# Performance work log

Measured on AMD Instinct MI355X. Metric: run time of the kernel, lower is better.

Reference implementation:

```python
import jax, jax.numpy as jnp
import numpy as np

# Config from Hyperparameters / __init__ args
B, S, D = 2, 2048, 512
H, KV, HD = 8, 4, 64          # num_heads, num_kv_heads, head_dim = D // H
ROPE_BASE = 10000.0
QK_GAIN_INIT = 1.5
EPS = 1e-6


def setup_inputs() -> dict:
    key = jax.random.key(0)
    k0, k1, k2, k3, k4 = jax.random.split(key, 5)
    std = 0.02
    return {
        "x": jax.random.normal(k0, (B, S, D), dtype=jnp.float32),
        "wq": jax.random.normal(k1, (H * HD, D), dtype=jnp.float32) * std,
        "wk": jax.random.normal(k2, (KV * HD, D), dtype=jnp.float32) * std,
        "wv": jax.random.normal(k3, (KV * HD, D), dtype=jnp.float32) * std,
        "wo": jax.random.normal(k4, (D, H * HD), dtype=jnp.float32) * std,
        "qk_gain": jnp.asarray(QK_GAIN_INIT, dtype=jnp.float32),
    }


def _rope_tables(seq_len, head_dim, base, dtype):
    inv_freq = 1.0 / (base ** (jnp.arange(0, head_dim, 2, dtype=jnp.float32) / head_dim))
    t = jnp.arange(seq_len, dtype=jnp.float32)
    freqs = t[:, None] * inv_freq[None, :]              # [S, HD/2]
    return jnp.cos(freqs).astype(dtype)[None, None], jnp.sin(freqs).astype(dtype)[None, None]


def _apply_rotary(x, cos, sin):
    # matches apply_rotary_emb: split halves, rotate
    half = x.shape[-1] // 2
    x1, x2 = x[..., :half], x[..., half:]
    return jnp.concatenate([x1 * cos + x2 * sin, x1 * (-sin) + x2 * cos], axis=-1)


def _rms_norm(u):
    return u * jax.lax.rsqrt(jnp.mean(u * u, axis=-1, keepdims=True) + EPS)


def reference(x, wq, wk, wv, wo, qk_gain):
    b, s, d = x.shape
    # fused-style QKV projections (CastedLinear, no bias)
    q = (x @ wq.T).reshape(b, s, H, HD).transpose(0, 2, 1, 3)    # [B,H,S,HD]
    k = (x @ wk.T).reshape(b, s, KV, HD).transpose(0, 2, 1, 3)   # [B,KV,S,HD]
    v = (x @ wv.T).reshape(b, s, KV, HD).transpose(0, 2, 1, 3)   # [B,KV,S,HD]

    cos, sin = _rope_tables(s, HD, ROPE_BASE, x.dtype)
    q = _apply_rotary(q, cos, sin)
    k = _apply_rotary(k, cos, sin)

    # QK RMS-norm with learnable gain (init 1.5) on q
    q = _rms_norm(q) * qk_gain
    k = _rms_norm(k)

    # GQA: expand KV heads to H query heads
    rep = H // KV
    k = jnp.repeat(k, rep, axis=1)   # [B,H,S,HD]
    v = jnp.repeat(v, rep, axis=1)

    scale = 1.0 / np.sqrt(HD)
    scores = jnp.einsum("bhqd,bhkd->bhqk", q, k) * scale         # [B,H,S,S]
    causal = jnp.tril(jnp.ones((s, s), dtype=bool))
    scores = jnp.where(causal, scores, jnp.finfo(scores.dtype).min)
    attn = jax.nn.softmax(scores, axis=-1)
    out = jnp.einsum("bhqk,bhkd->bhqd", attn, v)                 # [B,H,S,HD]
    out = out.transpose(0, 2, 1, 3).reshape(b, s, H * HD)
    return out @ wo.T
```

## Files before the change

### kernel.cpp

```cpp
#include <hip/hip_runtime.h>
#include <math.h>

#define B_ 2
#define S_ 2048
#define D_ 512
#define H_ 8
#define KV_ 4
#define HD_ 64

typedef __attribute__((ext_vector_type(8))) short bf16x8;
typedef __attribute__((ext_vector_type(4))) short bf16x4;
typedef __attribute__((ext_vector_type(4))) float f32x4;
typedef __attribute__((ext_vector_type(16))) float f32x16;
typedef __attribute__((ext_vector_type(4))) unsigned u32x4;

static __device__ __forceinline__ unsigned short f2bf(float f) {
    union { float f; unsigned u; } v; v.f = f;
    unsigned r = v.u + 0x7FFFu + ((v.u >> 16) & 1);
    return (unsigned short)(r >> 16);
}

__global__ __launch_bounds__(256) void convert_pack_kernel(
    const float* __restrict__ x, const float* __restrict__ wq, const float* __restrict__ wk,
    const float* __restrict__ wv, const float* __restrict__ wo,
    unsigned short* __restrict__ xb, unsigned short* __restrict__ wqkv_b,
    unsigned short* __restrict__ wo_b, float* __restrict__ cosT, float* __restrict__ sinT) {
    if (blockIdx.x >= 2816) {
        int idx = (blockIdx.x - 2816) * 256 + threadIdx.x;
        int s = idx >> 5;
        int i = idx & 31;
        float invf = 1.0f / powf(10000.0f, (float)(2 * i) / (float)HD_);
        double a = (double)((float)s * invf);
        cosT[idx] = (float)cos(a);
        sinT[idx] = (float)sin(a);
        return;
    }
    int i4 = blockIdx.x * blockDim.x + threadIdx.x;
    int e = i4 * 4;
    const float* src;
    unsigned short* dst;
    if (e < 2097152)      { src = x + e;               dst = xb + e; }
    else if (e < 2359296) { src = wq + (e - 2097152);  dst = wqkv_b + (e - 2097152); }
    else if (e < 2490368) { src = wk + (e - 2359296);  dst = wqkv_b + (e - 2097152); }
    else if (e < 2621440) { src = wv + (e - 2490368);  dst = wqkv_b + (e - 2097152); }
    else                  { src = wo + (e - 2621440);  dst = wo_b + (e - 2621440); }
    float4 v = *(const float4*)src;
    bf16x4 o;
    o[0] = (short)f2bf(v.x); o[1] = (short)f2bf(v.y);
    o[2] = (short)f2bf(v.z); o[3] = (short)f2bf(v.w);
    *(bf16x4*)dst = o;
}

template <int EPI, typename OutT>
static __device__ __forceinline__ void gemm_body(
    const unsigned short* __restrict__ A, const unsigned short* __restrict__ Bw,
    OutT* __restrict__ Y, int K, int ldy, int bn, int bm,
    unsigned short* As, unsigned short* Bs,
    const float* __restrict__ cosT, const float* __restrict__ sinT,
    const float* __restrict__ gainp) {
    const int t = threadIdx.x;
    const int w = t >> 6, l = t & 63;
    const int g = l >> 4, c = l & 15;
    const int wr = w >> 1, wc = w & 1;
    f32x4 acc[4][4] = {};
    const int lrow = l >> 2;
    const int lcol = (l & 3) * 8;
    for (int k0 = 0; k0 < K; k0 += 32) {
#pragma unroll
        for (int r = 0; r < 2; ++r) {
            int ci = w * 2 + r;
            const unsigned short* ga = A + (size_t)(bm + ci * 16 + lrow) * K + k0 + lcol;
            __builtin_amdgcn_global_load_lds(
                (const __attribute__((address_space(1))) void*)ga,
                (__attribute__((address_space(3))) void*)(As + ci * 512), 16, 0, 0);
            const unsigned short* gb = Bw + (size_t)(bn + ci * 16 + lrow) * K + k0 + lcol;
            __builtin_amdgcn_global_load_lds(
                (const __attribute__((address_space(1))) void*)gb,
                (__attribute__((address_space(3))) void*)(Bs + ci * 512), 16, 0, 0);
        }
        __syncthreads();
        bf16x8 av[4], bv[4];
#pragma unroll
        for (int i = 0; i < 4; ++i)
            av[i] = *(const bf16x8*)(As + (wr * 64 + i * 16 + c) * 32 + g * 8);
#pragma unroll
        for (int j = 0; j < 4; ++j)
            bv[j] = *(const bf16x8*)(Bs + (wc * 64 + j * 16 + c) * 32 + g * 8);
#pragma unroll
        for (int i = 0; i < 4; ++i)
#pragma unroll
            for (int j = 0; j < 4; ++j)
                acc[i][j] = __builtin_amdgcn_mfma_f32_16x16x32_bf16(av[i], bv[j], acc[i][j], 0, 0, 0);
        __syncthreads();
    }
    if constexpr (EPI == 2) {
        const float gv = *gainp;
        const float hscale = ((bn + wc * 64) < 512) ? gv : 1.0f;
#pragma unroll
        for (int i = 0; i < 4; ++i) {
#pragma unroll
            for (int r = 0; r < 4; ++r) {
                int row = bm + wr * 64 + i * 16 + g * 4 + r;
                int s = row & (S_ - 1);
                float c0 = cosT[s * 32 + c],      s0 = sinT[s * 32 + c];
                float c1 = cosT[s * 32 + c + 16], s1 = sinT[s * 32 + c + 16];
                float x1a = acc[i][0][r], x1b = acc[i][1][r];
                float x2a = acc[i][2][r], x2b = acc[i][3][r];
                float y1a = x1a * c0 + x2a * s0, y2a = x2a * c0 - x1a * s0;
                float y1b = x1b * c1 + x2b * s1, y2b = x2b * c1 - x1b * s1;
                float ss = y1a * y1a + y2a * y2a + y1b * y1b + y2b * y2b;
                ss += __shfl_xor(ss, 1, 64);
                ss += __shfl_xor(ss, 2, 64);
                ss += __shfl_xor(ss, 4, 64);
                ss += __shfl_xor(ss, 8, 64);
                float sc = rsqrtf(ss * (1.0f / 64.0f) + 1e-6f) * hscale;
                unsigned short* yr = (unsigned short*)Y + (size_t)row * ldy + bn + wc * 64 + c;
                yr[0]  = f2bf(y1a * sc);
                yr[16] = f2bf(y1b * sc);
                yr[32] = f2bf(y2a * sc);
                yr[48] = f2bf(y2b * sc);
            }
        }
    } else {
#pragma unroll
        for (int i = 0; i < 4; ++i)
#pragma unroll
            for (int j = 0; j < 4; ++j)
#pragma unroll
                for (int r = 0; r < 4; ++r) {
                    int row = bm + wr * 64 + i * 16 + g * 4 + r;
                    int col = bn + wc * 64 + j * 16 + c;
                    float v = acc[i][j][r];
                    if constexpr (EPI == 1)
                        Y[(size_t)row * ldy + col] = (OutT)f2bf(v);
                    else
                        Y[(size_t)row * ldy + col] = v;
                }
    }
}

__global__ __launch_bounds__(256) void gemm_proj_fused(
    const unsigned short* __restrict__ xb, const unsigned short* __restrict__ wqkv_b,
    unsigned short* __restrict__ qkv, unsigned short* __restrict__ vt,
    const float* __restrict__ cosT, const float* __restrict__ sinT,
    const float* __restrict__ gainp) {
    __shared__ unsigned short As[128 * 32];
    __shared__ unsigned short Bs[128 * 32];
    int bid = blockIdx.x;
    if (bid < 192) {
        int bx = bid % 6, by = bid / 6;
        gemm_body<2, unsigned short>(xb, wqkv_b, qkv, 512, 768, bx * 128, by * 128,
                                     As, Bs, cosT, sinT, gainp);
    } else {
        int b2 = bid - 192;
        int bx = b2 & 31, by = b2 >> 5;
        gemm_body<1, unsigned short>(wqkv_b + 768 * 512, xb, vt, 512, 4096, bx * 128, by * 128,
                                     As, Bs, nullptr, nullptr, nullptr);
    }
}

__global__ __launch_bounds__(256) void gemm_out(
    const unsigned short* __restrict__ A, const unsigned short* __restrict__ Bw,
    float* __restrict__ Y) {
    __shared__ unsigned short As[128 * 32];
    __shared__ unsigned short Bs[128 * 32];
    gemm_body<0, float>(A, Bw, Y, 512, 512, blockIdx.x % 4 * 128, blockIdx.x / 4 * 128,
                        As, Bs, nullptr, nullptr, nullptr);
}

#define SWZF(row) ((((row) + ((row) >> 3)) & 7) << 4)

__global__ __launch_bounds__(256, 3) void attn_mfma(const unsigned short* __restrict__ qkv,
                                                    const unsigned short* __restrict__ vt,
                                                    unsigned short* __restrict__ aout,
                                                    float* __restrict__ pO,
                                                    float* __restrict__ pL) {
    __shared__ alignas(128) char smem[32768];

    const int slot = blockIdx.x >> 4;
    const int bh = blockIdx.x & 15;
    int qt = 31, acc = 0;
    while (acc + (qt >> 3) + 1 <= slot) { acc += (qt >> 3) + 1; --qt; }
    const int part = slot - acc;
    const int np = (qt >> 3) + 1;
    const int kt0 = part * 8;
    const int kt1 = min(kt0 + 8, qt + 1);
    const int hh = bh & 7;
    const int b = bh >> 3;
    const int kvh = hh >> 1;

    const int t = threadIdx.x;
    const int w = t >> 6;
    const int l = t & 63;
    const int wq = w >> 1;
    const int wk = w & 1;
    const int hl = l >> 5;
    const int l31 = l & 31;

    const int row0 = t >> 3;
    const int row1 = (256 + t) >> 3;
    const int seg = l & 7;
    const int off0 = (seg * 16) ^ SWZF(row0);
    const int off1 = (seg * 16) ^ SWZF(row1);
    const int cb0 = w * 1024;
    const int cb1 = 4096 + w * 1024;

    bf16x8 qf[4];
    {
        const unsigned short* qrow =
            qkv + (size_t)(b * S_ + qt * 64 + wq * 32 + l31) * 768 + hh * 64 + hl * 8;
#pragma unroll
        for (int kd = 0; kd < 4; ++kd)
            qf[kd] = *(const bf16x8*)(qrow + kd * 16);
    }

    const char* kb = (const char*)qkv + ((size_t)(b * S_)) * 1536 + 1024 + kvh * 128;
    const char* vb = (const char*)vt + ((size_t)(kvh * 64)) * 8192 + (size_t)(b * S_) * 2;

#define STAGE(kt_, bufi_)                                                                        \
    do {                                                                                         \
        const char* ks_ = kb + (size_t)(kt_) * 64 * 1536;                                        \
        const char* vs_ = vb + (size_t)(kt_) * 128;                                              \
        char* kd_ = smem + (bufi_)*8192;                                                         \
        char* vd_ = smem + 16384 + (bufi_)*8192;                                                 \
        __builtin_amdgcn_global_load_lds(                                                        \
            (const __attribute__((address_space(1))) void*)(ks_ + (size_t)row0 * 1536 + off0),   \
            (__attribute__((address_space(3))) void*)(kd_ + cb0), 16, 0, 0);                     \
        __builtin_amdgcn_global_load_lds(                                                        \
            (const __attribute__((address_space(1))) void*)(ks_ + (size_t)row1 * 1536 + off1),   \
            (__attribute__((address_space(3))) void*)(kd_ + cb1), 16, 0, 0);                     \
        __builtin_amdgcn_global_load_lds(                                                        \
            (const __attribute__((address_space(1))) void*)(vs_ + (size_t)row0 * 8192 + off0),   \
            (__attribute__((address_space(3))) void*)(vd_ + cb0), 16, 0, 0);                     \
        __builtin_amdgcn_global_load_lds(                                                        \
            (const __attribute__((address_space(1))) void*)(vs_ + (size_t)row1 * 8192 + off1),   \
            (__attribute__((address_space(3))) void*)(vd_ + cb1), 16, 0, 0);                     \
    } while (0)

    STAGE(kt0, 0);
    __syncthreads();

    float l_part = 0.0f;
    f32x16 o_acc[2] = {};
    const float LS = 0.125f * 1.4426950408889634f;
    const float SH = 6.0f * 1.4426950408889634f;

    int buf = 0;
    for (int kt = kt0; kt < kt1; ++kt) {
        if (kt + 1 < kt1) STAGE(kt + 1, buf ^ 1);
        const char* KsB = smem + buf * 8192;
        const char* VtB = smem + 16384 + buf * 8192;
        const bool diag = (kt == qt);

        if (!(diag && wk > wq)) {
            f32x16 s_acc = {};
            {
                int arow = wk * 32 + l31;
                int af = SWZF(arow);
                __builtin_amdgcn_s_setprio(1);
#pragma unroll
                for (int kd = 0; kd < 4; ++kd) {
                    bf16x8 afr = *(const bf16x8*)(KsB + arow * 128 + ((kd * 32 + hl * 16) ^ af));
                    s_acc = __builtin_amdgcn_mfma_f32_32x32x16_bf16(afr, qf[kd], s_acc, 0, 0, 0);
                }
                __builtin_amdgcn_s_setprio(0);
            }
            bf16x8 vf[2][2];
#pragma unroll
            for (int nd = 0; nd < 2; ++nd) {
                int vr = nd * 32 + l31;
                int fv = SWZF(vr);
#pragma unroll
                for (int m = 0; m < 2; ++m)
                    vf[nd][m] = *(const bf16x8*)(VtB + vr * 128 + ((wk * 64 + m * 32 + hl * 16) ^ fv));
            }
            float p[16];
            if (diag && wk == wq) {
#pragma unroll
                for (int idx = 0; idx < 16; ++idx) {
                    int keyin = 4 * hl + 8 * (idx >> 2) + (idx & 3);
                    float e = exp2f(s_acc[idx] * LS - SH);
                    p[idx] = (keyin <= l31) ? e : 0.0f;
                }
            } else {
#pragma unroll
                for (int idx = 0; idx < 16; ++idx)
                    p[idx] = exp2f(s_acc[idx] * LS - SH);
            }
#pragma unroll
            for (int idx = 0; idx < 16; ++idx) l_part += p[idx];
            unsigned pw[8];
#pragma unroll
            for (int s = 0; s < 4; ++s)
#pragma unroll
                for (int j = 0; j < 2; ++j)
                    asm("v_cvt_pk_bf16_f32 %0, %1, %2"
                        : "=v"(pw[s * 2 + j])
                        : "v"(p[4 * s + 2 * j]), "v"(p[4 * s + 2 * j + 1]));
#pragma unroll
            for (int m = 0; m < 2; ++m) {
                asm volatile("v_permlane32_swap_b32 %0, %1" : "+v"(pw[4 * m + 0]), "+v"(pw[4 * m + 2]));
                asm volatile("v_permlane32_swap_b32 %0, %1" : "+v"(pw[4 * m + 1]), "+v"(pw[4 * m + 3]));
            }
            __builtin_amdgcn_s_setprio(1);
#pragma unroll
            for (int m = 0; m < 2; ++m) {
                u32x4 fu = {pw[4 * m + 0], pw[4 * m + 1], pw[4 * m + 2], pw[4 * m + 3]};
                bf16x8 pfr = *(bf16x8*)&fu;
#pragma unroll
                for (int nd = 0; nd < 2; ++nd)
                    o_acc[nd] = __builtin_amdgcn_mfma_f32_32x32x16_bf16(pfr, vf[nd][m], o_acc[nd], 0, 0, 0);
            }
            __builtin_amdgcn_s_setprio(0);
        }
        __syncthreads();
        buf ^= 1;
    }
#undef STAGE

    float* Os = (float*)smem;
    float* Ls = (float*)(smem + 16384);
    float lsum = l_part + __shfl_xor(l_part, 32, 64);
    if (hl == 0) Ls[wk * 64 + wq * 32 + l31] = lsum;
    if (wk == 0) {
#pragma unroll
        for (int nd = 0; nd < 2; ++nd)
#pragma unroll
            for (int reg = 0; reg < 16; ++reg) {
                int qrow = 4 * hl + 8 * (reg >> 2) + (reg & 3);
                Os[(wq * 32 + qrow) * 64 + nd * 32 + l31] = o_acc[nd][reg];
            }
    }
    __syncthreads();
    if (wk == 1) {
        if (np == 1) {
            unsigned short* ob = aout + ((size_t)(b * S_ + qt * 64 + wq * 32)) * 512 + hh * 64;
#pragma unroll
            for (int reg = 0; reg < 16; ++reg) {
                int qrow = 4 * hl + 8 * (reg >> 2) + (reg & 3);
                float ltot = Ls[wq * 32 + qrow] + Ls[64 + wq * 32 + qrow];
                float inv = __builtin_amdgcn_rcpf(ltot);
#pragma unroll
                for (int nd = 0; nd < 2; ++nd) {
                    float val = (o_acc[nd][reg] + Os[(wq * 32 + qrow) * 64 + nd * 32 + l31]) * inv;
                    ob[(size_t)qrow * 512 + nd * 32 + l31] = f2bf(val);
                }
            }
        } else {
            float* po = pO + (size_t)blockIdx.x * 4096;
            float* pl = pL + (size_t)blockIdx.x * 64;
#pragma unroll
            for (int reg = 0; reg < 16; ++reg) {
                int qrow = 4 * hl + 8 * (reg >> 2) + (reg & 3);
                float ltot = Ls[wq * 32 + qrow] + Ls[64 + wq * 32 + qrow];
                if (l31 == 0) pl[wq * 32 + qrow] = ltot;
#pragma unroll
                for (int nd = 0; nd < 2; ++nd)
                    po[(wq * 32 + qrow) * 64 + nd * 32 + l31] =
                        o_acc[nd][reg] + Os[(wq * 32 + qrow) * 64 + nd * 32 + l31];
            }
        }
    }
}

__global__ __launch_bounds__(256) void combine_kernel(const float* __restrict__ pO,
                                                      const float* __restrict__ pL,
                                                      unsigned short* __restrict__ aout) {
    const int cid = blockIdx.x;
    const int bh = cid & 15;
    const int qt = 31 - (cid >> 4);
    int qq = 31, acc = 0;
    while (qq > qt) { acc += (qq >> 3) + 1; --qq; }
    const int np = (qt >> 3) + 1;
    const int base = acc * 16 + bh;
    const int t = threadIdx.x;
    const int row = t >> 2;
    const int c0 = (t & 3) * 16;
    float l = 0.0f;
    float o[16] = {};
    for (int p = 0; p < np; ++p) {
        const int pid = base + p * 16;
        l += pL[(size_t)pid * 64 + row];
        const float* po = pO + (size_t)pid * 4096 + row * 64 + c0;
#pragma unroll
        for (int j4 = 0; j4 < 4; ++j4) {
            float4 v = *(const float4*)(po + j4 * 4);
            o[j4 * 4 + 0] += v.x; o[j4 * 4 + 1] += v.y;
            o[j4 * 4 + 2] += v.z; o[j4 * 4 + 3] += v.w;
        }
    }
    float inv = __builtin_amdgcn_rcpf(l);
    const int b = bh >> 3, hh = bh & 7;
    unsigned short* ob = aout + (size_t)(b * S_ + qt * 64 + row) * 512 + hh * 64 + c0;
    bf16x4 pk[4];
#pragma unroll
    for (int j4 = 0; j4 < 4; ++j4) {
        pk[j4][0] = (short)f2bf(o[j4 * 4 + 0] * inv);
        pk[j4][1] = (short)f2bf(o[j4 * 4 + 1] * inv);
        pk[j4][2] = (short)f2bf(o[j4 * 4 + 2] * inv);
        pk[j4][3] = (short)f2bf(o[j4 * 4 + 3] * inv);
        *(bf16x4*)(ob + j4 * 4) = pk[j4];
    }
}

extern "C" void kernel_launch(void* const* d_in, const int* in_sizes, int n_in,
                              void* d_out, int out_size, void* d_ws, size_t ws_size,
                              hipStream_t stream) {
    const float* x    = (const float*)d_in[0];
    const float* wq   = (const float*)d_in[1];
    const float* wk   = (const float*)d_in[2];
    const float* wv   = (const float*)d_in[3];
    const float* wo   = (const float*)d_in[4];
    const float* gain = (const float*)d_in[5];
    float* out = (float*)d_out;

    char* ws = (char*)d_ws;
    unsigned short* qkv    = (unsigned short*)(ws);
    unsigned short* vt     = (unsigned short*)(ws + (size_t)6  * 1024 * 1024);
    unsigned short* aout   = (unsigned short*)(ws + (size_t)8  * 1024 * 1024);
    unsigned short* xb     = (unsigned short*)(ws + (size_t)12 * 1024 * 1024);
    unsigned short* wqkv_b = (unsigned short*)(ws + (size_t)16 * 1024 * 1024);
    unsigned short* wo_b   = (unsigned short*)(ws + (size_t)17 * 1024 * 1024);
    float* cosT            = (float*)(ws + (size_t)18 * 1024 * 1024);
    float* sinT            = cosT + (size_t)S_ * (HD_ / 2);
    float* pO              = (float*)(ws + (size_t)32 * 1024 * 1024);
    float* pL              = pO + (size_t)1280 * 4096;

    convert_pack_kernel<<<3072, 256, 0, stream>>>(x, wq, wk, wv, wo, xb, wqkv_b, wo_b,
                                                  cosT, sinT);
    gemm_proj_fused<<<256, 256, 0, stream>>>(xb, wqkv_b, qkv, vt, cosT, sinT, gain);
    attn_mfma<<<1280, 256, 0, stream>>>(qkv, vt, aout, pO, pL);
    combine_kernel<<<384, 256, 0, stream>>>(pO, pL, aout);
    gemm_out<<<128, 256, 0, stream>>>(aout, wo_b, out);
}
```

Before: 68.23 us.

## Fuse split-K combine into attention via atomic counter last-block reduction

Removes the separate combine kernel. Each split attention block writes its partial O and L with agent-scope atomic stores, then bumps a per-(bh,qt) counter, and the last block to arrive reduces all partials and writes the bf16 output. The goal is to drop one kernel launch and its tail. In exchange it adds atomics, extra syncs and scalar (non-vectorized) relaxed loads and stores in the reduction path. It also relies on the counter being zeroed in the convert kernel.

```diff
diff --git a/kernel.cpp b/kernel.cpp
--- a/kernel.cpp
+++ b/kernel.cpp
@@ -24,8 +24,13 @@
     const float* __restrict__ x, const float* __restrict__ wq, const float* __restrict__ wk,
     const float* __restrict__ wv, const float* __restrict__ wo,
     unsigned short* __restrict__ xb, unsigned short* __restrict__ wqkv_b,
-    unsigned short* __restrict__ wo_b, float* __restrict__ cosT, float* __restrict__ sinT) {
+    unsigned short* __restrict__ wo_b, float* __restrict__ cosT, float* __restrict__ sinT,
+    int* __restrict__ cnt) {
     if (blockIdx.x >= 2816) {
+        if (blockIdx.x == 2816) {
+            cnt[threadIdx.x] = 0;
+            cnt[256 + threadIdx.x] = 0;
+        }
         int idx = (blockIdx.x - 2816) * 256 + threadIdx.x;
         int s = idx >> 5;
         int i = idx & 31;
@@ -174,14 +179,15 @@
                                                     const unsigned short* __restrict__ vt,
                                                     unsigned short* __restrict__ aout,
                                                     float* __restrict__ pO,
-                                                    float* __restrict__ pL) {
+                                                    float* __restrict__ pL,
+                                                    int* __restrict__ cnt) {
     __shared__ alignas(128) char smem[32768];
 
     const int slot = blockIdx.x >> 4;
     const int bh = blockIdx.x & 15;
-    int qt = 31, acc = 0;
-    while (acc + (qt >> 3) + 1 <= slot) { acc += (qt >> 3) + 1; --qt; }
-    const int part = slot - acc;
+    int qt = 31, sacc = 0;
+    while (sacc + (qt >> 3) + 1 <= slot) { sacc += (qt >> 3) + 1; --qt; }
+    const int part = slot - sacc;
     const int np = (qt >> 3) + 1;
     const int kt0 = part * 8;
     const int kt1 = min(kt0 + 8, qt + 1);
@@ -353,53 +359,48 @@
             for (int reg = 0; reg < 16; ++reg) {
                 int qrow = 4 * hl + 8 * (reg >> 2) + (reg & 3);
                 float ltot = Ls[wq * 32 + qrow] + Ls[64 + wq * 32 + qrow];
-                if (l31 == 0) pl[wq * 32 + qrow] = ltot;
-#pragma unroll
-                for (int nd = 0; nd < 2; ++nd)
-                    po[(wq * 32 + qrow) * 64 + nd * 32 + l31] =
-                        o_acc[nd][reg] + Os[(wq * 32 + qrow) * 64 + nd * 32 + l31];
-            }
-        }
-    }
-}
-
-__global__ __launch_bounds__(256) void combine_kernel(const float* __restrict__ pO,
-                                                      const float* __restrict__ pL,
-                                                      unsigned short* __restrict__ aout) {
-    const int cid = blockIdx.x;
-    const int bh = cid & 15;
-    const int qt = 31 - (cid >> 4);
-    int qq = 31, acc = 0;
-    while (qq > qt) { acc += (qq >> 3) + 1; --qq; }
-    const int np = (qt >> 3) + 1;
-    const int base = acc * 16 + bh;
-    const int t = threadIdx.x;
-    const int row = t >> 2;
-    const int c0 = (t & 3) * 16;
-    float l = 0.0f;
-    float o[16] = {};
-    for (int p = 0; p < np; ++p) {
-        const int pid = base + p * 16;
-        l += pL[(size_t)pid * 64 + row];
-        const float* po = pO + (size_t)pid * 4096 + row * 64 + c0;
-#pragma unroll
-        for (int j4 = 0; j4 < 4; ++j4) {
-            float4 v = *(const float4*)(po + j4 * 4);
-            o[j4 * 4 + 0] += v.x; o[j4 * 4 + 1] += v.y;
-            o[j4 * 4 + 2] += v.z; o[j4 * 4 + 3] += v.w;
-        }
-    }
-    float inv = __builtin_amdgcn_rcpf(l);
-    const int b = bh >> 3, hh = bh & 7;
-    unsigned short* ob = aout + (size_t)(b * S_ + qt * 64 + row) * 512 + hh * 64 + c0;
-    bf16x4 pk[4];
-#pragma unroll
-    for (int j4 = 0; j4 < 4; ++j4) {
-        pk[j4][0] = (short)f2bf(o[j4 * 4 + 0] * inv);
-        pk[j4][1] = (short)f2bf(o[j4 * 4 + 1] * inv);
-        pk[j4][2] = (short)f2bf(o[j4 * 4 + 2] * inv);
-        pk[j4][3] = (short)f2bf(o[j4 * 4 + 3] * inv);
-        *(bf16x4*)(ob + j4 * 4) = pk[j4];
+                if (l31 == 0)
+                    __hip_atomic_store(&pl[wq * 32 + qrow], ltot,
+                                       __ATOMIC_RELAXED, __HIP_MEMORY_SCOPE_AGENT);
+#pragma unroll
+                for (int nd = 0; nd < 2; ++nd) {
+                    float val = o_acc[nd][reg] + Os[(wq * 32 + qrow) * 64 + nd * 32 + l31];
+                    __hip_atomic_store(&po[(wq * 32 + qrow) * 64 + nd * 32 + l31], val,
+                                       __ATOMIC_RELAXED, __HIP_MEMORY_SCOPE_AGENT);
+                }
+            }
+        }
+    }
+
+    if (np > 1) {
+        __syncthreads();
+        int* flagp = (int*)(smem + 16896);
+        if (t == 0) {
+            int old = __hip_atomic_fetch_add(&cnt[bh * 32 + qt], 1,
+                                             __ATOMIC_ACQ_REL, __HIP_MEMORY_SCOPE_AGENT);
+            *flagp = (old == np - 1) ? 1 : 0;
+        }
+        __syncthreads();
+        if (*flagp) {
+            const int row = t >> 2;
+            const int c0 = (t & 3) * 16;
+            float ltot = 0.0f;
+            float o[16] = {};
+            for (int p = 0; p < np; ++p) {
+                const int pid = (sacc + p) * 16 + bh;
+                ltot += __hip_atomic_load(&pL[(size_t)pid * 64 + row],
+                                          __ATOMIC_RELAXED, __HIP_MEMORY_SCOPE_AGENT);
+                const float* po2 = pO + (size_t)pid * 4096 + row * 64 + c0;
+#pragma unroll
+                for (int j = 0; j < 16; ++j)
+                    o[j] += __hip_atomic_load(&po2[j], __ATOMIC_RELAXED, __HIP_MEMORY_SCOPE_AGENT);
+            }
+            float inv = __builtin_amdgcn_rcpf(ltot);
+            unsigned short* ob = aout + (size_t)(b * S_ + qt * 64 + row) * 512 + hh * 64 + c0;
+#pragma unroll
+            for (int j = 0; j < 16; ++j)
+                ob[j] = f2bf(o[j] * inv);
+        }
     }
 }
 
@@ -423,13 +424,13 @@
     unsigned short* wo_b   = (unsigned short*)(ws + (size_t)17 * 1024 * 1024);
     float* cosT            = (float*)(ws + (size_t)18 * 1024 * 1024);
     float* sinT            = cosT + (size_t)S_ * (HD_ / 2);
+    int*   cnt             = (int*)(ws + (size_t)31 * 1024 * 1024);
     float* pO              = (float*)(ws + (size_t)32 * 1024 * 1024);
     float* pL              = pO + (size_t)1280 * 4096;
 
     convert_pack_kernel<<<3072, 256, 0, stream>>>(x, wq, wk, wv, wo, xb, wqkv_b, wo_b,
-                                                  cosT, sinT);
+                                                  cosT, sinT, cnt);
     gemm_proj_fused<<<256, 256, 0, stream>>>(xb, wqkv_b, qkv, vt, cosT, sinT, gain);
-    attn_mfma<<<1280, 256, 0, stream>>>(qkv, vt, aout, pO, pL);
-    combine_kernel<<<384, 256, 0, stream>>>(pO, pL, aout);
+    attn_mfma<<<1280, 256, 0, stream>>>(qkv, vt, aout, pO, pL, cnt);
     gemm_out<<<128, 256, 0, stream>>>(aout, wo_b, out);
 }
```

New measurement: 103.6 us. 51.8% more time.

## Load K/V fragments directly from global memory instead of LDS double-buffering

Applied to the files above, without the earlier changes.

The attention kernel no longer stages K and V^T tiles into shared memory with async global_load_lds double-buffering and per-tile barriers. Each wave now loads its MFMA operand fragments straight from global memory, and the causal-diagonal skip becomes a plain continue. Shared memory shrinks to what the epilogue reduction needs and launch bounds rise to 4 blocks per CU to raise occupancy. In exchange, K/V data is re-read by several waves through L1/L2, and the explicit prefetch overlap with compute is lost.

```diff
diff --git a/kernel.cpp b/kernel.cpp
--- a/kernel.cpp
+++ b/kernel.cpp
@@ -168,14 +168,12 @@
                         As, Bs, nullptr, nullptr, nullptr);
 }
 
-#define SWZF(row) ((((row) + ((row) >> 3)) & 7) << 4)
-
-__global__ __launch_bounds__(256, 3) void attn_mfma(const unsigned short* __restrict__ qkv,
+__global__ __launch_bounds__(256, 4) void attn_mfma(const unsigned short* __restrict__ qkv,
                                                     const unsigned short* __restrict__ vt,
                                                     unsigned short* __restrict__ aout,
                                                     float* __restrict__ pO,
                                                     float* __restrict__ pL) {
-    __shared__ alignas(128) char smem[32768];
+    __shared__ alignas(128) char smem[16896];
 
     const int slot = blockIdx.x >> 4;
     const int bh = blockIdx.x & 15;
@@ -197,14 +195,6 @@
     const int hl = l >> 5;
     const int l31 = l & 31;
 
-    const int row0 = t >> 3;
-    const int row1 = (256 + t) >> 3;
-    const int seg = l & 7;
-    const int off0 = (seg * 16) ^ SWZF(row0);
-    const int off1 = (seg * 16) ^ SWZF(row1);
-    const int cb0 = w * 1024;
-    const int cb1 = 4096 + w * 1024;
-
     bf16x8 qf[4];
     {
         const unsigned short* qrow =
@@ -214,109 +204,77 @@
             qf[kd] = *(const bf16x8*)(qrow + kd * 16);
     }
 
-    const char* kb = (const char*)qkv + ((size_t)(b * S_)) * 1536 + 1024 + kvh * 128;
-    const char* vb = (const char*)vt + ((size_t)(kvh * 64)) * 8192 + (size_t)(b * S_) * 2;
-
-#define STAGE(kt_, bufi_)                                                                        \
-    do {                                                                                         \
-        const char* ks_ = kb + (size_t)(kt_) * 64 * 1536;                                        \
-        const char* vs_ = vb + (size_t)(kt_) * 128;                                              \
-        char* kd_ = smem + (bufi_)*8192;                                                         \
-        char* vd_ = smem + 16384 + (bufi_)*8192;                                                 \
-        __builtin_amdgcn_global_load_lds(                                                        \
-            (const __attribute__((address_space(1))) void*)(ks_ + (size_t)row0 * 1536 + off0),   \
-            (__attribute__((address_space(3))) void*)(kd_ + cb0), 16, 0, 0);                     \
-        __builtin_amdgcn_global_load_lds(                                                        \
-            (const __attribute__((address_space(1))) void*)(ks_ + (size_t)row1 * 1536 + off1),   \
-            (__attribute__((address_space(3))) void*)(kd_ + cb1), 16, 0, 0);                     \
-        __builtin_amdgcn_global_load_lds(                                                        \
-            (const __attribute__((address_space(1))) void*)(vs_ + (size_t)row0 * 8192 + off0),   \
-            (__attribute__((address_space(3))) void*)(vd_ + cb0), 16, 0, 0);                     \
-        __builtin_amdgcn_global_load_lds(                                                        \
-            (const __attribute__((address_space(1))) void*)(vs_ + (size_t)row1 * 8192 + off1),   \
-            (__attribute__((address_space(3))) void*)(vd_ + cb1), 16, 0, 0);                     \
-    } while (0)
-
-    STAGE(kt0, 0);
-    __syncthreads();
+    const unsigned short* kp = qkv + (size_t)(b * S_) * 768 + 512 + kvh * 64;
+    const unsigned short* vp = vt + (size_t)(kvh * 64) * 4096 + b * S_;
 
     float l_part = 0.0f;
     f32x16 o_acc[2] = {};
     const float LS = 0.125f * 1.4426950408889634f;
     const float SH = 6.0f * 1.4426950408889634f;
 
-    int buf = 0;
     for (int kt = kt0; kt < kt1; ++kt) {
-        if (kt + 1 < kt1) STAGE(kt + 1, buf ^ 1);
-        const char* KsB = smem + buf * 8192;
-        const char* VtB = smem + 16384 + buf * 8192;
         const bool diag = (kt == qt);
-
-        if (!(diag && wk > wq)) {
-            f32x16 s_acc = {};
-            {
-                int arow = wk * 32 + l31;
-                int af = SWZF(arow);
-                __builtin_amdgcn_s_setprio(1);
-#pragma unroll
-                for (int kd = 0; kd < 4; ++kd) {
-                    bf16x8 afr = *(const bf16x8*)(KsB + arow * 128 + ((kd * 32 + hl * 16) ^ af));
-                    s_acc = __builtin_amdgcn_mfma_f32_32x32x16_bf16(afr, qf[kd], s_acc, 0, 0, 0);
-                }
-                __builtin_amdgcn_s_setprio(0);
-            }
-            bf16x8 vf[2][2];
-#pragma unroll
-            for (int nd = 0; nd < 2; ++nd) {
-                int vr = nd * 32 + l31;
-                int fv = SWZF(vr);
-#pragma unroll
-                for (int m = 0; m < 2; ++m)
-                    vf[nd][m] = *(const bf16x8*)(VtB + vr * 128 + ((wk * 64 + m * 32 + hl * 16) ^ fv));
-            }
-            float p[16];
-            if (diag && wk == wq) {
-#pragma unroll
-                for (int idx = 0; idx < 16; ++idx) {
-                    int keyin = 4 * hl + 8 * (idx >> 2) + (idx & 3);
-                    float e = exp2f(s_acc[idx] * LS - SH);
-                    p[idx] = (keyin <= l31) ? e : 0.0f;
-                }
-            } else {
-#pragma unroll
-                for (int idx = 0; idx < 16; ++idx)
-                    p[idx] = exp2f(s_acc[idx] * LS - SH);
-            }
-#pragma unroll
-            for (int idx = 0; idx < 16; ++idx) l_part += p[idx];
-            unsigned pw[8];
-#pragma unroll
-            for (int s = 0; s < 4; ++s)
-#pragma unroll
-                for (int j = 0; j < 2; ++j)
-                    asm("v_cvt_pk_bf16_f32 %0, %1, %2"
-                        : "=v"(pw[s * 2 + j])
-                        : "v"(p[4 * s + 2 * j]), "v"(p[4 * s + 2 * j + 1]));
-#pragma unroll
-            for (int m = 0; m < 2; ++m) {
-                asm volatile("v_permlane32_swap_b32 %0, %1" : "+v"(pw[4 * m + 0]), "+v"(pw[4 * m + 2]));
-                asm volatile("v_permlane32_swap_b32 %0, %1" : "+v"(pw[4 * m + 1]), "+v"(pw[4 * m + 3]));
-            }
-            __builtin_amdgcn_s_setprio(1);
-#pragma unroll
-            for (int m = 0; m < 2; ++m) {
-                u32x4 fu = {pw[4 * m + 0], pw[4 * m + 1], pw[4 * m + 2], pw[4 * m + 3]};
-                bf16x8 pfr = *(bf16x8*)&fu;
-#pragma unroll
-                for (int nd = 0; nd < 2; ++nd)
-                    o_acc[nd] = __builtin_amdgcn_mfma_f32_32x32x16_bf16(pfr, vf[nd][m], o_acc[nd], 0, 0, 0);
-            }
-            __builtin_amdgcn_s_setprio(0);
-        }
-        __syncthreads();
-        buf ^= 1;
-    }
-#undef STAGE
+        if (diag && wk > wq) continue;
+
+        const unsigned short* krow = kp + (size_t)(kt * 64 + wk * 32 + l31) * 768 + hl * 8;
+        f32x16 s_acc = {};
+        __builtin_amdgcn_s_setprio(1);
+#pragma unroll
+        for (int kd = 0; kd < 4; ++kd) {
+            bf16x8 afr = *(const bf16x8*)(krow + kd * 16);
+            s_acc = __builtin_amdgcn_mfma_f32_32x32x16_bf16(afr, qf[kd], s_acc, 0, 0, 0);
+        }
+        __builtin_amdgcn_s_setprio(0);
+
+        bf16x8 vf[2][2];
+#pragma unroll
+        for (int nd = 0; nd < 2; ++nd)
+#pragma unroll
+            for (int m = 0; m < 2; ++m)
+                vf[nd][m] = *(const bf16x8*)(vp + (size_t)(nd * 32 + l31) * 4096 +
+                                             kt * 64 + wk * 32 + m * 16 + hl * 8);
+
+        float p[16];
+        if (diag && wk == wq) {
+#pragma unroll
+            for (int idx = 0; idx < 16; ++idx) {
+                int keyin = 4 * hl + 8 * (idx >> 2) + (idx & 3);
+                float e = exp2f(s_acc[idx] * LS - SH);
+                p[idx] = (keyin <= l31) ? e : 0.0f;
+            }
+        } else {
+#pragma unroll
+            for (int idx = 0; idx < 16; ++idx)
+                p[idx] = exp2f(s_acc[idx] * LS - SH);
+        }
+#pragma unroll
+        for (int idx = 0; idx < 16; ++idx) l_part += p[idx];
+
+        unsigned pw[8];
+#pragma unroll
+        for (int s = 0; s < 4; ++s)
+#pragma unroll
+            for (int j = 0; j < 2; ++j)
+                asm("v_cvt_pk_bf16_f32 %0, %1, %2"
+                    : "=v"(pw[s * 2 + j])
+                    : "v"(p[4 * s + 2 * j]), "v"(p[4 * s + 2 * j + 1]));
+#pragma unroll
+        for (int m = 0; m < 2; ++m) {
+            asm volatile("v_permlane32_swap_b32 %0, %1" : "+v"(pw[4 * m + 0]), "+v"(pw[4 * m + 2]));
+            asm volatile("v_permlane32_swap_b32 %0, %1" : "+v"(pw[4 * m + 1]), "+v"(pw[4 * m + 3]));
+        }
+
+        __builtin_amdgcn_s_setprio(1);
+#pragma unroll
+        for (int m = 0; m < 2; ++m) {
+            u32x4 fu = {pw[4 * m + 0], pw[4 * m + 1], pw[4 * m + 2], pw[4 * m + 3]};
+            bf16x8 pfr = *(bf16x8*)&fu;
+#pragma unroll
+            for (int nd = 0; nd < 2; ++nd)
+                o_acc[nd] = __builtin_amdgcn_mfma_f32_32x32x16_bf16(pfr, vf[nd][m], o_acc[nd], 0, 0, 0);
+        }
+        __builtin_amdgcn_s_setprio(0);
+    }
 
     float* Os = (float*)smem;
     float* Ls = (float*)(smem + 16384);
```

Result: slower. 93.06 us (+36.4%).
